# Kernel tuning notes

Measured on AMD Instinct MI355X. Metric: run time of the kernel, lower is better.

Reference implementation:

```python
import jax, jax.numpy as jnp
import numpy as np
import math

B, S, D, H = 1, 2048, 2048, 16
DH = D // H  # 128
HALF = DH // 2  # 64


def setup_inputs() -> dict:
    key = jax.random.key(0)
    ks = jax.random.split(key, 6)
    x = jax.random.normal(ks[0], (B, S, D), dtype=jnp.float32)
    # rotary frequencies: freqs_cis = exp(i * t * theta), theta_j = 10000^{-2j/DH}
    inv_freq = 1.0 / (10000.0 ** (np.arange(0, DH, 2, dtype=np.float32) / DH))  # [HALF]
    t = np.arange(S, dtype=np.float32)
    angles = np.outer(t, inv_freq)  # [S, HALF]
    freqs_cos = jnp.asarray(np.cos(angles), dtype=jnp.float32)
    freqs_sin = jnp.asarray(np.sin(angles), dtype=jnp.float32)
    # additive causal mask [1,1,S,S]
    mask = jnp.triu(jnp.full((S, S), -1e9, dtype=jnp.float32), k=1)[None, None]
    scale = 0.02
    wq = jax.random.normal(ks[1], (D, D), dtype=jnp.float32) * scale
    wk = jax.random.normal(ks[2], (D, D), dtype=jnp.float32) * scale
    wv = jax.random.normal(ks[3], (D, D), dtype=jnp.float32) * scale
    wo = jax.random.normal(ks[4], (D, D), dtype=jnp.float32) * scale
    return {"x": x, "freqs_cos": freqs_cos, "freqs_sin": freqs_sin, "mask": mask,
            "wq": wq, "wk": wk, "wv": wv, "wo": wo, "start_pos": 0}


def _apply_rope(t, cos, sin):
    # t: [B,S,H,DH]; cos/sin: [S,HALF] broadcast as [1,S,1,HALF]
    tr = t.reshape(*t.shape[:-1], HALF, 2)
    even, odd = tr[..., 0], tr[..., 1]
    c = cos[None, :, None, :]
    s = sin[None, :, None, :]
    out_even = even * c - odd * s
    out_odd = even * s + odd * c
    return jnp.stack([out_even, out_odd], axis=-1).reshape(t.shape)


def reference(x, freqs_cos, freqs_sin, mask, wq, wk, wv, wo, start_pos):
    bsz, seqlen, _ = x.shape
    q = (x @ wq.T).reshape(bsz, seqlen, H, DH)
    k = (x @ wk.T).reshape(bsz, seqlen, H, DH)
    v = (x @ wv.T).reshape(bsz, seqlen, H, DH)
    q = _apply_rope(q, freqs_cos, freqs_sin)
    k = _apply_rope(k, freqs_cos, freqs_sin)
    q = q.transpose(0, 2, 1, 3)  # [B,H,S,DH]
    k = k.transpose(0, 2, 1, 3)
    v = v.transpose(0, 2, 1, 3)
    scores = jnp.einsum('bhqd,bhkd->bhqk', q, k) / math.sqrt(DH) + mask
    probs = jax.nn.softmax(scores, axis=-1)
    out = jnp.einsum('bhqk,bhkd->bhqd', probs, v)  # [B,H,S,DH]
    # faithful to original: transpose(2,3) then view(bsz, seqlen, dim)
    out = out.transpose(0, 1, 3, 2).reshape(bsz, seqlen, D)
    return out @ wo.T
```

## Files before the change

### kernel.cpp

```cpp
#include <hip/hip_runtime.h>

typedef unsigned short u16;
typedef unsigned int   u32;
typedef short  short8   __attribute__((ext_vector_type(8)));
typedef float  floatx4  __attribute__((ext_vector_type(4)));
typedef u16    ushortx2 __attribute__((ext_vector_type(2)));
typedef u16    ushortx4 __attribute__((ext_vector_type(4)));

__device__ __forceinline__ float bf2f(u16 u) {
  union { u32 i; float f; } v; v.i = ((u32)u) << 16; return v.f;
}
__device__ __forceinline__ u16 f2bf(float x) {
  union { float f; u32 i; } v; v.f = x;
  u32 r = v.i + 0x7FFFu + ((v.i >> 16) & 1u);
  return (u16)(r >> 16);
}

#if __has_builtin(__builtin_amdgcn_exp2f)
#define EXP2F(x) __builtin_amdgcn_exp2f(x)
#else
#define EXP2F(x) __exp2f(x)
#endif

#define GLOAD_LDS16(gptr, lptr)                                                   \
  __builtin_amdgcn_global_load_lds(                                               \
      (const __attribute__((address_space(1))) void*)(gptr),                      \
      (__attribute__((address_space(3))) void*)(lptr), 16, 0, 0)

#define WAITV(n) asm volatile("s_waitcnt vmcnt(" #n ")" ::: "memory")
#define WAITL    asm volatile("s_waitcnt lgkmcnt(0)" ::: "memory")
#define BAR      __builtin_amdgcn_s_barrier()

__global__ __launch_bounds__(256) void cvt_all(
    const floatx4* __restrict__ x,  const floatx4* __restrict__ wq,
    const floatx4* __restrict__ wk, const floatx4* __restrict__ wv,
    const floatx4* __restrict__ wo,
    ushortx4* __restrict__ xb, ushortx4* __restrict__ wqkv,
    ushortx4* __restrict__ wob) {
  int i = blockIdx.x * 256 + threadIdx.x;
  const floatx4* in; ushortx4* out;
  switch (blockIdx.y) {
    case 0:  in = x;  out = xb; break;
    case 1:  in = wq; out = wqkv; break;
    case 2:  in = wk; out = wqkv + (size_t)1048576; break;
    case 3:  in = wv; out = wqkv + (size_t)2097152; break;
    default: in = wo; out = wob; break;
  }
  floatx4 v = in[i];
  ushortx4 o;
  o.x = f2bf(v.x); o.y = f2bf(v.y); o.z = f2bf(v.z); o.w = f2bf(v.w);
  out[i] = o;
}

__global__ __launch_bounds__(512, 2) void gemm256_bt(
    const u16* __restrict__ A, const u16* __restrict__ B, u16* __restrict__ C,
    int N, int K, int lda, int ldb, int ldc) {
  const int cpx = gridDim.x >> 3;
  const int wg = ((int)blockIdx.x & 7) * cpx + ((int)blockIdx.x >> 3);
  const int ntn = N / 192;
  const int m0 = (wg / ntn) << 8;
  const int n0 = (wg % ntn) * 192;

  __shared__ __align__(16) u16 As[2][256][64];
  __shared__ __align__(16) u16 Bs[2][192][64];

  const int t = threadIdx.x;
  const int lane = t & 63;
  const int wave = t >> 6;
  const int wr = wave >> 2;
  const int wc = wave & 3;
  const int quad = lane >> 4;
  const int mrow = lane & 15;
  const int sw = mrow & 7;

  const int srow = lane >> 3;
  const int gso  = ((lane & 7) ^ srow) << 3;

  const u16* gA = A + (size_t)(m0 + (wave << 3) + srow) * lda + gso;
  const u16* gB = B + (size_t)(n0 + (wave << 3) + srow) * ldb + gso;

  floatx4 acc[8][3] = {};
  short8 afr[4][2], bfr[3][2];

  const int NT = K >> 6;

#define ST_A(nb, h, kt)                                                        \
  do {                                                                         \
    GLOAD_LDS16(gA + (size_t)((h) * 128) * lda + ((kt) << 6),                  \
                &As[nb][(h) * 128 + (wave << 3)][0]);                          \
    GLOAD_LDS16(gA + (size_t)((h) * 128 + 64) * lda + ((kt) << 6),             \
                &As[nb][(h) * 128 + 64 + (wave << 3)][0]);                     \
  } while (0)
#define ST_B1(nb, c, kt)                                                       \
  do {                                                                         \
    GLOAD_LDS16(gB + (size_t)((c) * 64) * ldb + ((kt) << 6),                   \
                &Bs[nb][(c) * 64 + (wave << 3)][0]);                           \
  } while (0)

#define LDA4(bf, base_row)                                                     \
  do {                                                                         \
    _Pragma("unroll") for (int i_ = 0; i_ < 4; i_++)                           \
      _Pragma("unroll") for (int kk_ = 0; kk_ < 2; kk_++)                      \
        afr[i_][kk_] = *(const short8*)&As[bf][(base_row) + (i_ << 4) + mrow]  \
                            [(((kk_ << 2) | quad) ^ sw) << 3];                 \
  } while (0)
#define LDB1(bf, j)                                                            \
  do {                                                                         \
    _Pragma("unroll") for (int kk_ = 0; kk_ < 2; kk_++)                        \
      bfr[j][kk_] = *(const short8*)&Bs[bf][(j) * 64 + (wc << 4) + mrow]       \
          [(((kk_ << 2) | quad) ^ sw) << 3];                                   \
  } while (0)
#define MMQ8(ilo, j)                                                           \
  do {                                                                         \
    __builtin_amdgcn_s_setprio(1);                                             \
    _Pragma("unroll") for (int kk_ = 0; kk_ < 2; kk_++)                        \
      _Pragma("unroll") for (int i_ = 0; i_ < 4; i_++)                         \
        acc[(ilo) + i_][j] = __builtin_amdgcn_mfma_f32_16x16x32_bf16(          \
            afr[i_][kk_], bfr[j][kk_], acc[(ilo) + i_][j], 0, 0, 0);           \
    __builtin_amdgcn_s_setprio(0);                                             \
  } while (0)

  ST_A(0, 0, 0); ST_B1(0, 0, 0); ST_B1(0, 1, 0); ST_B1(0, 2, 0); ST_A(0, 1, 0);
  WAITV(3);
  BAR;

  for (int kt = 0; kt < NT - 1; kt++) {
    const int bf = kt & 1, nb = bf ^ 1;
    LDA4(bf, (wr << 6));
    LDB1(bf, 0);
    LDB1(bf, 1);
    ST_A(nb, 0, kt + 1);
    ST_B1(nb, 0, kt + 1);
    WAITV(3);
    BAR;
    MMQ8(0, 0);
    MMQ8(0, 1);
    LDB1(bf, 2);
    ST_B1(nb, 1, kt + 1);
    ST_B1(nb, 2, kt + 1);
    BAR;
    MMQ8(0, 2);
    LDA4(bf, 128 + (wr << 6));
    MMQ8(4, 0);
    ST_A(nb, 1, kt + 1);
    WAITV(3);
    BAR;
    MMQ8(4, 1);
    MMQ8(4, 2);
  }
  {
    const int bf = (NT - 1) & 1;
    LDA4(bf, (wr << 6));
    LDB1(bf, 0);
    LDB1(bf, 1);
    WAITV(0);
    BAR;
    MMQ8(0, 0);
    MMQ8(0, 1);
    LDB1(bf, 2);
    BAR;
    MMQ8(0, 2);
    LDA4(bf, 128 + (wr << 6));
    MMQ8(4, 0);
    BAR;
    MMQ8(4, 1);
    MMQ8(4, 2);
  }

#pragma unroll
  for (int i = 0; i < 8; i++) {
    int row0 = m0 + ((i >= 4) ? 128 : 0) + (wr << 6) + ((i & 3) << 4) + (quad << 2);
#pragma unroll
    for (int j = 0; j < 3; j++) {
      int col = n0 + j * 64 + (wc << 4) + mrow;
#pragma unroll
      for (int r = 0; r < 4; r++)
        C[(size_t)(row0 + r) * ldc + col] = f2bf(acc[i][j][r]);
    }
  }
#undef ST_A
#undef ST_B1
#undef LDA4
#undef LDB1
#undef MMQ8
}

__global__ __launch_bounds__(256) void gemm_bt(
    const u16* __restrict__ A, const u16* __restrict__ B, void* __restrict__ Cv,
    int M, int N, int K, int lda, int ldb, int ldc,
    long batchA, long batchB, long batchC, int outBF16) {
  const int m0 = blockIdx.y << 7;
  const int n0 = blockIdx.x << 7;

  A += (long)blockIdx.z * batchA;
  B += (long)blockIdx.z * batchB;
  const long cbase = (long)blockIdx.z * batchC;

  __shared__ __align__(16) u16 As[128][64];
  __shared__ __align__(16) u16 Bs[128][64];

  const int t = threadIdx.x;
  const int lane = t & 63;
  const int wave = t >> 6;
  const int wm = (wave >> 1) << 6;
  const int wn = (wave & 1) << 6;
  const int quad = lane >> 4;
  const int mrow = lane & 15;
  const int sw8 = mrow & 7;

  floatx4 acc[4][4] = {};

  const int srow = lane >> 3;
  const int gseg = (((lane & 7) ^ srow) << 3);
  const u16* gA = A + (long)(m0 + (wave << 5) + srow) * lda + gseg;
  const u16* gB = B + (long)(n0 + (wave << 5) + srow) * ldb + gseg;

  for (int k0 = 0; k0 < K; k0 += 64) {
    __syncthreads();
#pragma unroll
    for (int ii = 0; ii < 4; ii++) {
      GLOAD_LDS16(gA + k0 + (size_t)(ii << 3) * lda, &As[(wave << 5) + (ii << 3)][0]);
      GLOAD_LDS16(gB + k0 + (size_t)(ii << 3) * ldb, &Bs[(wave << 5) + (ii << 3)][0]);
    }
    __syncthreads();

#pragma unroll
    for (int kh = 0; kh < 2; kh++) {
      const int sidx = ((kh << 2) | quad) ^ sw8;
      short8 af[4], bfr[4];
#pragma unroll
      for (int i = 0; i < 4; i++)
        af[i] = *(const short8*)&As[wm + (i << 4) + mrow][sidx << 3];
#pragma unroll
      for (int j = 0; j < 4; j++)
        bfr[j] = *(const short8*)&Bs[wn + (j << 4) + mrow][sidx << 3];
#pragma unroll
      for (int i = 0; i < 4; i++)
#pragma unroll
        for (int j = 0; j < 4; j++)
          acc[i][j] = __builtin_amdgcn_mfma_f32_16x16x32_bf16(af[i], bfr[j], acc[i][j], 0, 0, 0);
    }
  }

#pragma unroll
  for (int i = 0; i < 4; i++) {
    int row0 = m0 + wm + (i << 4) + (quad << 2);
#pragma unroll
    for (int j = 0; j < 4; j++) {
      int col = n0 + wn + (j << 4) + mrow;
#pragma unroll
      for (int r = 0; r < 4; r++) {
        long idx = cbase + (long)(row0 + r) * ldc + col;
        float val = acc[i][j][r];
        if (outBF16) ((u16*)Cv)[idx] = f2bf(val);
        else         ((float*)Cv)[idx] = val;
      }
    }
  }
}

__global__ __launch_bounds__(256) void transpose_v(const u16* __restrict__ src,
                                                   u16* __restrict__ dst) {
  __shared__ u16 tile[64][68];
  const int d0 = blockIdx.x << 6;
  const int s0 = blockIdx.y << 6;
  const int tx = (threadIdx.x & 15) << 2;
  const int ty = threadIdx.x >> 4;
#pragma unroll
  for (int rr = 0; rr < 64; rr += 16) {
    ushortx4 v = *(const ushortx4*)(src + (size_t)(s0 + ty + rr) * 6144 + d0 + tx);
    *(ushortx4*)&tile[ty + rr][tx] = v;
  }
  __syncthreads();
#pragma unroll
  for (int rr = 0; rr < 64; rr += 16) {
    int r = ty + rr;
    ushortx4 o;
    o.x = tile[tx + 0][r]; o.y = tile[tx + 1][r];
    o.z = tile[tx + 2][r]; o.w = tile[tx + 3][r];
    *(ushortx4*)(dst + (size_t)(d0 + r) * 2048 + s0 + tx) = o;
  }
}

__global__ __launch_bounds__(256) void rope_qk(u16* __restrict__ qkv,
                                               const float* __restrict__ cs,
                                               const float* __restrict__ sn) {
  int idx = blockIdx.x * 256 + threadIdx.x;
  int p = idx & 63;
  int h = (idx >> 6) & 15;
  int s = idx >> 10;
  float c  = cs[(s << 6) | p];
  float si = sn[(s << 6) | p];
  float scale = blockIdx.y ? 1.0f : 0.12751743f;
  size_t off = (size_t)s * 6144 + (blockIdx.y ? 2048 : 0) + (h << 7) + (p << 1);
  ushortx2 eo = *(ushortx2*)(qkv + off);
  float e = bf2f(eo.x), o = bf2f(eo.y);
  ushortx2 r;
  r.x = f2bf((e * c - o * si) * scale);
  r.y = f2bf((e * si + o * c) * scale);
  *(ushortx2*)(qkv + off) = r;
}

__global__ __launch_bounds__(256, 2) void flash_attn(
    const u16* __restrict__ QKVp, const u16* __restrict__ VTp,
    u16* __restrict__ ATp) {
  const int r0id = (int)blockIdx.x + ((int)blockIdx.y << 5);
  const int h    = r0id & 15;
  const int qsub = 31 - (r0id >> 4);
  const int q0 = qsub << 6;
  const int ktmax = qsub >> 1;

  __shared__ __align__(16) u16 Ks[128][128];
  __shared__ __align__(16) u16 Vs[128][128];
  __shared__ __align__(16) u16 Ps[64][128];

  const int t = threadIdx.x;
  const int lane = t & 63;
  const int wave = t >> 6;
  const int quad = lane >> 4;
  const int mrow = lane & 15;
  const int sw   = mrow & 7;
  const int wmS = (wave & 1) << 5;
  const int wnS = (wave >> 1) << 6;
  const int wmV = (wave >> 1) << 6;
  const int wnP = (wave & 1) << 5;

  const int r4  = lane >> 4;
  const int seg = lane & 15;
  const int c0 = ((seg ^ r4) << 3);
  const int c4 = ((seg ^ (r4 + 4)) << 3);

  const u16* qbase = QKVp + (size_t)q0 * 6144 + (h << 7);
  const u16* kbase = QKVp + 2048 + (h << 7);
  const u16* vbase = VTp + (size_t)(h << 7) * 2048;

#define STAGE_K(kt)                                                            \
  do {                                                                         \
    int rr0_ = wave << 5;                                                      \
    _Pragma("unroll") for (int ii_ = 0; ii_ < 8; ii_++) {                      \
      int rr_ = rr0_ + (ii_ << 2);                                             \
      GLOAD_LDS16(kbase + (size_t)(((kt) << 7) + rr_ + r4) * 6144 +            \
                      ((ii_ & 1) ? c4 : c0),                                   \
                  &Ks[rr_][0]);                                                \
    }                                                                          \
  } while (0)
#define STAGE_V(kt)                                                            \
  do {                                                                         \
    int rr0_ = wave << 5;                                                      \
    _Pragma("unroll") for (int ii_ = 0; ii_ < 8; ii_++) {                      \
      int rr_ = rr0_ + (ii_ << 2);                                             \
      GLOAD_LDS16(vbase + (size_t)(rr_ + r4) * 2048 + ((kt) << 7) +            \
                      ((ii_ & 1) ? c4 : c0),                                   \
                  &Vs[rr_][0]);                                                \
    }                                                                          \
  } while (0)

  short8 aq[2][4];
#pragma unroll
  for (int i = 0; i < 2; i++)
#pragma unroll
    for (int kk = 0; kk < 4; kk++)
      aq[i][kk] = *(const short8*)(qbase + (size_t)(wmS + (i << 4) + mrow) * 6144 +
                                   (kk << 5) + (quad << 3));

  const short8 ones = {0x3F80, 0x3F80, 0x3F80, 0x3F80,
                       0x3F80, 0x3F80, 0x3F80, 0x3F80};

  floatx4 Oa[4][2] = {};
  floatx4 Oa1[2] = {};

  const float C2 = 23.083120654223414f;

  STAGE_K(0);
  STAGE_V(0);
  WAITV(8);
  BAR;

  for (int kt = 0; kt <= ktmax; kt++) {
    floatx4 sa[2][4] = {};
#pragma unroll
    for (int kk = 0; kk < 4; kk++) {
      short8 bk[4];
#pragma unroll
      for (int j = 0; j < 4; j++)
        bk[j] = *(const short8*)&Ks[wnS + (j << 4) + mrow][(((kk << 2) | quad) ^ sw) << 3];
      __builtin_amdgcn_s_setprio(1);
#pragma unroll
      for (int i = 0; i < 2; i++)
#pragma unroll
        for (int j = 0; j < 4; j++)
          sa[i][j] = __builtin_amdgcn_mfma_f32_16x16x32_bf16(aq[i][kk], bk[j], sa[i][j], 0, 0, 0);
      __builtin_amdgcn_s_setprio(0);
    }
    if (kt == ktmax) {
#pragma unroll
      for (int i = 0; i < 2; i++)
#pragma unroll
        for (int j = 0; j < 4; j++)
#pragma unroll
          for (int r = 0; r < 4; r++) {
            int ql = q0 + wmS + (i << 4) + (quad << 2) + r;
            int sl = (kt << 7) + wnS + (j << 4) + mrow;
            if (sl > ql) sa[i][j][r] = -1e30f;
          }
    }
#pragma unroll
    for (int i = 0; i < 2; i++)
#pragma unroll
      for (int j = 0; j < 4; j++)
#pragma unroll
        for (int r = 0; r < 4; r++) {
          int row = wmS + (i << 4) + (quad << 2) + r;
          int col = wnS + (j << 4) + mrow;
          Ps[row][((((col >> 3) ^ (row & 7)) << 3) | (col & 7))] =
              f2bf(EXP2F(sa[i][j][r] - C2));
        }
    WAITV(0);
    WAITL;
    BAR;

    if (kt < ktmax) STAGE_K(kt + 1);

#pragma unroll
    for (int kk = 0; kk < 4; kk++) {
      short8 av[4], bp[2];
#pragma unroll
      for (int i = 0; i < 4; i++)
        av[i] = *(const short8*)&Vs[wmV + (i << 4) + mrow][(((kk << 2) | quad) ^ sw) << 3];
#pragma unroll
      for (int j = 0; j < 2; j++)
        bp[j] = *(const short8*)&Ps[wnP + (j << 4) + mrow][(((kk << 2) | quad) ^ sw) << 3];
      __builtin_amdgcn_s_setprio(1);
#pragma unroll
      for (int i = 0; i < 4; i++)
#pragma unroll
        for (int j = 0; j < 2; j++)
          Oa[i][j] = __builtin_amdgcn_mfma_f32_16x16x32_bf16(av[i], bp[j], Oa[i][j], 0, 0, 0);
#pragma unroll
      for (int j = 0; j < 2; j++)
        Oa1[j] = __builtin_amdgcn_mfma_f32_16x16x32_bf16(ones, bp[j], Oa1[j], 0, 0, 0);
      __builtin_amdgcn_s_setprio(0);
    }
    WAITL;
    BAR;

    if (kt < ktmax) STAGE_V(kt + 1);
    WAITV(8);
    BAR;
  }
#undef STAGE_K
#undef STAGE_V

  float linv[2];
#pragma unroll
  for (int j = 0; j < 2; j++) linv[j] = 1.f / Oa1[j][0];
#pragma unroll
  for (int i = 0; i < 4; i++) {
    int drow = (h << 7) + wmV + (i << 4) + (quad << 2);
#pragma unroll
    for (int j = 0; j < 2; j++) {
      int col = q0 + wnP + (j << 4) + mrow;
#pragma unroll
      for (int r = 0; r < 4; r++)
        ATp[(size_t)(drow + r) * 2048 + col] = f2bf(Oa[i][j][r] * linv[j]);
    }
  }
}

__global__ __launch_bounds__(256) void reduce2(const floatx4* __restrict__ a,
                                               const floatx4* __restrict__ b,
                                               floatx4* __restrict__ o) {
  int i = blockIdx.x * 256 + threadIdx.x;
  o[i] = a[i] + b[i];
}

extern "C" void kernel_launch(void* const* d_in, const int* in_sizes, int n_in,
                              void* d_out, int out_size, void* d_ws, size_t ws_size,
                              hipStream_t stream) {
  const float* x  = (const float*)d_in[0];
  const float* fc = (const float*)d_in[1];
  const float* fs = (const float*)d_in[2];
  const float* wq = (const float*)d_in[4];
  const float* wk = (const float*)d_in[5];
  const float* wv = (const float*)d_in[6];
  const float* wo = (const float*)d_in[7];
  float* out = (float*)d_out;

  char* ws = (char*)d_ws;
  const size_t MB = 1024 * 1024;
  u16*   XB   = (u16*)(ws + 0 * MB);
  u16*   WQKV = (u16*)(ws + 8 * MB);
  u16*   WOb  = (u16*)(ws + 32 * MB);
  u16*   QKV  = (u16*)(ws + 40 * MB);
  u16*   VT   = (u16*)(ws + 64 * MB);
  u16*   AT   = (u16*)(ws + 72 * MB);
  float* PART = (float*)(ws + 80 * MB);

  int use_split = (ws_size >= 113 * MB);

  dim3 blk(256);
  cvt_all<<<dim3(4096, 5), blk, 0, stream>>>(
      (const floatx4*)x, (const floatx4*)wq, (const floatx4*)wk,
      (const floatx4*)wv, (const floatx4*)wo,
      (ushortx4*)XB, (ushortx4*)WQKV, (ushortx4*)WOb);

  gemm256_bt<<<dim3(256), dim3(512), 0, stream>>>(XB, WQKV, QKV,
                                                  6144, 2048, 2048, 2048, 6144);

  transpose_v<<<dim3(32, 32), blk, 0, stream>>>(QKV + 4096, VT);
  rope_qk<<<dim3(8192, 2), blk, 0, stream>>>(QKV, fc, fs);

  flash_attn<<<dim3(32, 16), blk, 0, stream>>>(QKV, VT, AT);

  if (use_split) {
    gemm_bt<<<dim3(16, 16, 2), blk, 0, stream>>>(AT, WOb, PART, 2048, 2048, 1024,
                                                 2048, 2048, 2048,
                                                 1024, 1024, (long)2048 * 2048, 0);
    reduce2<<<4096, blk, 0, stream>>>((const floatx4*)PART,
                                      (const floatx4*)(PART + (size_t)2048 * 2048),
                                      (floatx4*)out);
  } else {
    gemm_bt<<<dim3(16, 16, 1), blk, 0, stream>>>(AT, WOb, out, 2048, 2048, 2048,
                                                 2048, 2048, 2048, 0, 0, 0, 0);
  }
}
```

Measured before the change: 275.9 us.

## Pipeline output GEMM with double-buffered LDS, drop split-K, fuse rope and V transpose

Swaps the split-K output projection plus its reduce kernel for a single-pass GEMM that double-buffers A/B tiles in LDS. It prefetches the next k-tile with async global-to-LDS loads while MFMAs run, raises scheduling priority around the MFMA blocks, and remaps workgroups for cache locality. Separately, the rope and V-transpose kernels are merged into one launch to save launch overhead. The cost is only 256 workgroups for the output GEMM with no split-K, and it relies on the WAITV/BAR macros from the existing code.

```diff
diff --git a/kernel.cpp b/kernel.cpp
--- a/kernel.cpp
+++ b/kernel.cpp
@@ -185,120 +185,162 @@
 #undef MMQ8
 }
 
-__global__ __launch_bounds__(256) void gemm_bt(
-    const u16* __restrict__ A, const u16* __restrict__ B, void* __restrict__ Cv,
-    int M, int N, int K, int lda, int ldb, int ldc,
-    long batchA, long batchB, long batchC, int outBF16) {
-  const int m0 = blockIdx.y << 7;
-  const int n0 = blockIdx.x << 7;
-
-  A += (long)blockIdx.z * batchA;
-  B += (long)blockIdx.z * batchB;
-  const long cbase = (long)blockIdx.z * batchC;
-
-  __shared__ __align__(16) u16 As[128][64];
-  __shared__ __align__(16) u16 Bs[128][64];
+__global__ __launch_bounds__(256, 2) void gemm_out(
+    const u16* __restrict__ A, const u16* __restrict__ B,
+    float* __restrict__ C) {
+  const int wg = ((int)blockIdx.x & 7) * 32 + ((int)blockIdx.x >> 3);
+  const int m0 = (wg >> 4) << 7;
+  const int n0 = (wg & 15) << 7;
+
+  __shared__ __align__(16) u16 As[2][128][64];
+  __shared__ __align__(16) u16 Bs[2][128][64];
 
   const int t = threadIdx.x;
   const int lane = t & 63;
   const int wave = t >> 6;
-  const int wm = (wave >> 1) << 6;
-  const int wn = (wave & 1) << 6;
+  const int wr = wave >> 1;
+  const int wc = wave & 1;
   const int quad = lane >> 4;
   const int mrow = lane & 15;
-  const int sw8 = mrow & 7;
+  const int sw = mrow & 7;
+
+  const int srow = lane >> 3;
+  const int gso  = ((lane & 7) ^ srow) << 3;
+
+  const u16* gA = A + (size_t)(m0 + (wave << 3) + srow) * 2048 + gso;
+  const u16* gB = B + (size_t)(n0 + (wave << 3) + srow) * 2048 + gso;
 
   floatx4 acc[4][4] = {};
-
-  const int srow = lane >> 3;
-  const int gseg = (((lane & 7) ^ srow) << 3);
-  const u16* gA = A + (long)(m0 + (wave << 5) + srow) * lda + gseg;
-  const u16* gB = B + (long)(n0 + (wave << 5) + srow) * ldb + gseg;
-
-  for (int k0 = 0; k0 < K; k0 += 64) {
+  short8 afr[4][2], bfr[4][2];
+
+  const int NT = 32;
+
+#define OST_A(nb, p, kt)                                                       \
+  GLOAD_LDS16(gA + (size_t)((p) * 32) * 2048 + ((kt) << 6),                    \
+              &As[nb][(p) * 32 + (wave << 3)][0])
+#define OST_B(nb, p, kt)                                                       \
+  GLOAD_LDS16(gB + (size_t)((p) * 32) * 2048 + ((kt) << 6),                    \
+              &Bs[nb][(p) * 32 + (wave << 3)][0])
+
+#define OLDA(bf)                                                               \
+  do {                                                                         \
+    _Pragma("unroll") for (int i_ = 0; i_ < 4; i_++)                           \
+      _Pragma("unroll") for (int kk_ = 0; kk_ < 2; kk_++)                      \
+        afr[i_][kk_] = *(const short8*)&As[bf][(wr << 6) + (i_ << 4) + mrow]   \
+                            [(((kk_ << 2) | quad) ^ sw) << 3];                 \
+  } while (0)
+#define OLDB2(bf, jlo)                                                         \
+  do {                                                                         \
+    _Pragma("unroll") for (int j_ = 0; j_ < 2; j_++)                           \
+      _Pragma("unroll") for (int kk_ = 0; kk_ < 2; kk_++)                      \
+        bfr[(jlo) + j_][kk_] =                                                 \
+            *(const short8*)&Bs[bf][(wc << 6) + (((jlo) + j_) << 4) + mrow]    \
+                [(((kk_ << 2) | quad) ^ sw) << 3];                             \
+  } while (0)
+#define OMM16(jlo)                                                             \
+  do {                                                                         \
+    __builtin_amdgcn_s_setprio(1);                                             \
+    _Pragma("unroll") for (int kk_ = 0; kk_ < 2; kk_++)                        \
+      _Pragma("unroll") for (int i_ = 0; i_ < 4; i_++)                         \
+        _Pragma("unroll") for (int j_ = 0; j_ < 2; j_++)                       \
+          acc[i_][(jlo) + j_] = __builtin_amdgcn_mfma_f32_16x16x32_bf16(       \
+              afr[i_][kk_], bfr[(jlo) + j_][kk_], acc[i_][(jlo) + j_], 0, 0, 0);\
+    __builtin_amdgcn_s_setprio(0);                                             \
+  } while (0)
+
+  OST_A(0, 0, 0); OST_A(0, 1, 0); OST_A(0, 2, 0); OST_A(0, 3, 0);
+  OST_B(0, 0, 0); OST_B(0, 2, 0); OST_B(0, 1, 0); OST_B(0, 3, 0);
+  WAITV(2);
+  BAR;
+
+  for (int kt = 0; kt < NT - 1; kt++) {
+    const int bf = kt & 1, nb = bf ^ 1;
+    OLDA(bf);
+    OLDB2(bf, 0);
+    OST_A(nb, 0, kt + 1); OST_A(nb, 1, kt + 1);
+    OST_A(nb, 2, kt + 1); OST_A(nb, 3, kt + 1);
+    OST_B(nb, 0, kt + 1); OST_B(nb, 2, kt + 1);
+    WAITV(6);
+    BAR;
+    OMM16(0);
+    OLDB2(bf, 2);
+    OST_B(nb, 1, kt + 1); OST_B(nb, 3, kt + 1);
+    WAITV(2);
+    BAR;
+    OMM16(2);
+  }
+  {
+    const int bf = (NT - 1) & 1;
+    OLDA(bf);
+    OLDB2(bf, 0);
+    WAITV(0);
+    BAR;
+    OMM16(0);
+    OLDB2(bf, 2);
+    OMM16(2);
+  }
+
+#pragma unroll
+  for (int i = 0; i < 4; i++) {
+    int row0 = m0 + (wr << 6) + (i << 4) + (quad << 2);
+#pragma unroll
+    for (int j = 0; j < 4; j++) {
+      int col = n0 + (wc << 6) + (j << 4) + mrow;
+#pragma unroll
+      for (int r = 0; r < 4; r++)
+        C[(size_t)(row0 + r) * 2048 + col] = acc[i][j][r];
+    }
+  }
+#undef OST_A
+#undef OST_B
+#undef OLDA
+#undef OLDB2
+#undef OMM16
+}
+
+__global__ __launch_bounds__(256) void rope_trans(
+    u16* __restrict__ qkv, const float* __restrict__ cs,
+    const float* __restrict__ sn, u16* __restrict__ vt) {
+  __shared__ u16 tile[64][68];
+  const int bx = blockIdx.x;
+  if (bx < 16384) {
+    const int isK = bx >> 13;
+    int idx = (bx & 8191) * 256 + threadIdx.x;
+    int p = idx & 63;
+    int h = (idx >> 6) & 15;
+    int s = idx >> 10;
+    float c  = cs[(s << 6) | p];
+    float si = sn[(s << 6) | p];
+    float scale = isK ? 1.0f : 0.12751743f;
+    size_t off = (size_t)s * 6144 + (isK ? 2048 : 0) + (h << 7) + (p << 1);
+    ushortx2 eo = *(ushortx2*)(qkv + off);
+    float e = bf2f(eo.x), o = bf2f(eo.y);
+    ushortx2 r;
+    r.x = f2bf((e * c - o * si) * scale);
+    r.y = f2bf((e * si + o * c) * scale);
+    *(ushortx2*)(qkv + off) = r;
+  } else {
+    const int b = bx - 16384;
+    const u16* src = qkv + 4096;
+    const int d0 = (b & 31) << 6;
+    const int s0 = (b >> 5) << 6;
+    const int tx = (threadIdx.x & 15) << 2;
+    const int ty = threadIdx.x >> 4;
+#pragma unroll
+    for (int rr = 0; rr < 64; rr += 16) {
+      ushortx4 v = *(const ushortx4*)(src + (size_t)(s0 + ty + rr) * 6144 + d0 + tx);
+      *(ushortx4*)&tile[ty + rr][tx] = v;
+    }
     __syncthreads();
 #pragma unroll
-    for (int ii = 0; ii < 4; ii++) {
-      GLOAD_LDS16(gA + k0 + (size_t)(ii << 3) * lda, &As[(wave << 5) + (ii << 3)][0]);
-      GLOAD_LDS16(gB + k0 + (size_t)(ii << 3) * ldb, &Bs[(wave << 5) + (ii << 3)][0]);
-    }
-    __syncthreads();
-
-#pragma unroll
-    for (int kh = 0; kh < 2; kh++) {
-      const int sidx = ((kh << 2) | quad) ^ sw8;
-      short8 af[4], bfr[4];
-#pragma unroll
-      for (int i = 0; i < 4; i++)
-        af[i] = *(const short8*)&As[wm + (i << 4) + mrow][sidx << 3];
-#pragma unroll
-      for (int j = 0; j < 4; j++)
-        bfr[j] = *(const short8*)&Bs[wn + (j << 4) + mrow][sidx << 3];
-#pragma unroll
-      for (int i = 0; i < 4; i++)
-#pragma unroll
-        for (int j = 0; j < 4; j++)
-          acc[i][j] = __builtin_amdgcn_mfma_f32_16x16x32_bf16(af[i], bfr[j], acc[i][j], 0, 0, 0);
-    }
-  }
-
-#pragma unroll
-  for (int i = 0; i < 4; i++) {
-    int row0 = m0 + wm + (i << 4) + (quad << 2);
-#pragma unroll
-    for (int j = 0; j < 4; j++) {
-      int col = n0 + wn + (j << 4) + mrow;
-#pragma unroll
-      for (int r = 0; r < 4; r++) {
-        long idx = cbase + (long)(row0 + r) * ldc + col;
-        float val = acc[i][j][r];
-        if (outBF16) ((u16*)Cv)[idx] = f2bf(val);
-        else         ((float*)Cv)[idx] = val;
-      }
-    }
-  }
-}
-
-__global__ __launch_bounds__(256) void transpose_v(const u16* __restrict__ src,
-                                                   u16* __restrict__ dst) {
-  __shared__ u16 tile[64][68];
-  const int d0 = blockIdx.x << 6;
-  const int s0 = blockIdx.y << 6;
-  const int tx = (threadIdx.x & 15) << 2;
-  const int ty = threadIdx.x >> 4;
-#pragma unroll
-  for (int rr = 0; rr < 64; rr += 16) {
-    ushortx4 v = *(const ushortx4*)(src + (size_t)(s0 + ty + rr) * 6144 + d0 + tx);
-    *(ushortx4*)&tile[ty + rr][tx] = v;
-  }
-  __syncthreads();
-#pragma unroll
-  for (int rr = 0; rr < 64; rr += 16) {
-    int r = ty + rr;
-    ushortx4 o;
-    o.x = tile[tx + 0][r]; o.y = tile[tx + 1][r];
-    o.z = tile[tx + 2][r]; o.w = tile[tx + 3][r];
-    *(ushortx4*)(dst + (size_t)(d0 + r) * 2048 + s0 + tx) = o;
-  }
-}
-
-__global__ __launch_bounds__(256) void rope_qk(u16* __restrict__ qkv,
-                                               const float* __restrict__ cs,
-                                               const float* __restrict__ sn) {
-  int idx = blockIdx.x * 256 + threadIdx.x;
-  int p = idx & 63;
-  int h = (idx >> 6) & 15;
-  int s = idx >> 10;
-  float c  = cs[(s << 6) | p];
-  float si = sn[(s << 6) | p];
-  float scale = blockIdx.y ? 1.0f : 0.12751743f;
-  size_t off = (size_t)s * 6144 + (blockIdx.y ? 2048 : 0) + (h << 7) + (p << 1);
-  ushortx2 eo = *(ushortx2*)(qkv + off);
-  float e = bf2f(eo.x), o = bf2f(eo.y);
-  ushortx2 r;
-  r.x = f2bf((e * c - o * si) * scale);
-  r.y = f2bf((e * si + o * c) * scale);
-  *(ushortx2*)(qkv + off) = r;
+    for (int rr = 0; rr < 64; rr += 16) {
+      int r = ty + rr;
+      ushortx4 o;
+      o.x = tile[tx + 0][r]; o.y = tile[tx + 1][r];
+      o.z = tile[tx + 2][r]; o.w = tile[tx + 3][r];
+      *(ushortx4*)(vt + (size_t)(d0 + r) * 2048 + s0 + tx) = o;
+    }
+  }
 }
 
 __global__ __launch_bounds__(256, 2) void flash_attn(
@@ -465,13 +507,6 @@
         ATp[(size_t)(drow + r) * 2048 + col] = f2bf(Oa[i][j][r] * linv[j]);
     }
   }
-}
-
-__global__ __launch_bounds__(256) void reduce2(const floatx4* __restrict__ a,
-                                               const floatx4* __restrict__ b,
-                                               floatx4* __restrict__ o) {
-  int i = blockIdx.x * 256 + threadIdx.x;
-  o[i] = a[i] + b[i];
 }
 
 extern "C" void kernel_launch(void* const* d_in, const int* in_sizes, int n_in,
@@ -494,9 +529,6 @@
   u16*   QKV  = (u16*)(ws + 40 * MB);
   u16*   VT   = (u16*)(ws + 64 * MB);
   u16*   AT   = (u16*)(ws + 72 * MB);
-  float* PART = (float*)(ws + 80 * MB);
-
-  int use_split = (ws_size >= 113 * MB);
 
   dim3 blk(256);
   cvt_all<<<dim3(4096, 5), blk, 0, stream>>>(
@@ -507,20 +539,9 @@
   gemm256_bt<<<dim3(256), dim3(512), 0, stream>>>(XB, WQKV, QKV,
                                                   6144, 2048, 2048, 2048, 6144);
 
-  transpose_v<<<dim3(32, 32), blk, 0, stream>>>(QKV + 4096, VT);
-  rope_qk<<<dim3(8192, 2), blk, 0, stream>>>(QKV, fc, fs);
+  rope_trans<<<dim3(17408), blk, 0, stream>>>(QKV, fc, fs, VT);
 
   flash_attn<<<dim3(32, 16), blk, 0, stream>>>(QKV, VT, AT);
 
-  if (use_split) {
-    gemm_bt<<<dim3(16, 16, 2), blk, 0, stream>>>(AT, WOb, PART, 2048, 2048, 1024,
-                                                 2048, 2048, 2048,
-                                                 1024, 1024, (long)2048 * 2048, 0);
-    reduce2<<<4096, blk, 0, stream>>>((const floatx4*)PART,
-                                      (const floatx4*)(PART + (size_t)2048 * 2048),
-                                      (floatx4*)out);
-  } else {
-    gemm_bt<<<dim3(16, 16, 1), blk, 0, stream>>>(AT, WOb, out, 2048, 2048, 2048,
-                                                 2048, 2048, 2048, 0, 0, 0, 0);
-  }
-}
+  gemm_out<<<dim3(256), blk, 0, stream>>>(AT, WOb, out);
+}
```

New measurement: 266.7 us. -3.3%, faster.
